# Optimization experiments

Hardware: AMD Instinct MI355X
Metric: run time of the kernel (lower is better)

Reference implementation:

```python
import jax, jax.numpy as jnp
import numpy as np

B = 131072
LATENT, COND = 32, 96
HIDDEN, OUT = 128, 64
E = 8            # num experts
NUM_LAYER = 3    # hidden layer count -> NUM_LAYER+1 expert layers
GH = 128         # gate hidden size
INPUT = LATENT + COND      # 128
INTER = LATENT + HIDDEN    # 160
EPS = 1e-5


def _u(key, shape, stdv):
    return jax.random.uniform(key, shape, jnp.float32, -stdv, stdv)


def setup_inputs() -> dict:
    key = jax.random.key(0)
    ks = jax.random.split(key, 20)
    inp = {
        'z': jax.random.normal(ks[0], (B, LATENT), jnp.float32),
        'c': jax.random.normal(ks[1], (B, COND), jnp.float32),
    }
    # expert layers: (in_dim, out_dim) per layer
    dims = [(INPUT, HIDDEN), (INTER, HIDDEN), (INTER, HIDDEN), (INTER, OUT)]
    for i, (j, k) in enumerate(dims):
        stdv = 1.0 / np.sqrt(j)
        inp[f'w{i}'] = _u(ks[2 + 2 * i], (E, j, k), stdv)
        inp[f'b{i}'] = _u(ks[3 + 2 * i], (E, k), stdv)
    # gate MLP: Linear(INPUT,GH) -> ELU -> Linear(GH,GH) -> ELU -> Linear(GH,E)
    gd = [(INPUT, GH), (GH, GH), (GH, E)]
    for i, (j, k) in enumerate(gd):
        stdv = 1.0 / np.sqrt(j)
        inp[f'gw{i}'] = _u(ks[10 + 2 * i], (j, k), stdv)
        inp[f'gb{i}'] = _u(ks[11 + 2 * i], (k,), stdv)
    return inp


def _layernorm(x):
    # F.layer_norm(x, x.shape[1:]) with no affine params
    mu = jnp.mean(x, axis=-1, keepdims=True)
    var = jnp.mean(jnp.square(x - mu), axis=-1, keepdims=True)
    return (x - mu) * jax.lax.rsqrt(var + EPS)


def reference(z, c, w0, b0, w1, b1, w2, b2, w3, b3,
              gw0, gb0, gw1, gb1, gw2, gb2):
    x = jnp.concatenate([z, c], axis=-1)                      # [B, INPUT]
    h = jax.nn.elu(x @ gw0 + gb0)
    h = jax.nn.elu(h @ gw1 + gb1)
    coeff = jax.nn.softmax(h @ gw2 + gb2, axis=-1)            # [B, E]

    layer_out = c
    layers = [(w0, b0, True), (w1, b1, True), (w2, b2, True), (w3, b3, False)]
    for w, b, act in layers:
        inp = jnp.concatenate([z, layer_out], axis=-1)        # [B, J]
        inp = _layernorm(inp)
        mixed_bias = coeff @ b                                # be,ek->bk
        mixed = jnp.einsum('be,bj,ejk->bk', coeff, inp, w)    # soft-MoE mix
        out = mixed + mixed_bias
        layer_out = jax.nn.elu(out) if act else out
    return layer_out
```

## Files before the change

### kernel.cpp

```cpp
#include <hip/hip_runtime.h>

typedef _Float16 f16;
typedef _Float16 f16x2 __attribute__((ext_vector_type(2)));
typedef _Float16 f16x4 __attribute__((ext_vector_type(4)));
typedef _Float16 f16x8 __attribute__((ext_vector_type(8)));
typedef float f32x16 __attribute__((ext_vector_type(16)));

#define DEV __device__ __forceinline__
#define MFMA16(a, b, cc) __builtin_amdgcn_mfma_f32_32x32x16_f16(a, b, cc, 0, 0, 0)


constexpr int OFF_W0 = 0;
constexpr int OFF_W1 = 131072;
constexpr int OFF_W2 = 294912;
constexpr int OFF_W3 = 458752;
constexpr int OFF_G0 = 540672;
constexpr int OFF_G1 = 557056;
constexpr int OFF_B0 = 573440;
constexpr int OFF_B1 = 575488;
constexpr int OFF_B2 = 577536;
constexpr int OFF_B3 = 579584;

__global__ __launch_bounds__(256) void repack_kernel(
    const float* __restrict__ w0, const float* __restrict__ w1,
    const float* __restrict__ w2, const float* __restrict__ w3,
    const float* __restrict__ gw0, const float* __restrict__ gw1,
    const float* __restrict__ b0, const float* __restrict__ b1,
    const float* __restrict__ b2, const float* __restrict__ b3,
    f16* __restrict__ ws)
{
  int g = blockIdx.x * 256 + threadIdx.x;
  if (g < 71680) {
    const float* src; int S, CT, K, dstoff, lg;
    if (g < 16384)      { src = w0;  S = 8;  CT = 4; K = 128; dstoff = OFF_W0; lg = g; }
    else if (g < 36864) { src = w1;  S = 10; CT = 4; K = 128; dstoff = OFF_W1; lg = g - 16384; }
    else if (g < 57344) { src = w2;  S = 10; CT = 4; K = 128; dstoff = OFF_W2; lg = g - 36864; }
    else if (g < 67584) { src = w3;  S = 10; CT = 2; K = 64;  dstoff = OFF_W3; lg = g - 57344; }
    else if (g < 69632) { src = gw0; S = 8;  CT = 4; K = 128; dstoff = OFF_G0; lg = g - 67584; }
    else                { src = gw1; S = 8;  CT = 4; K = 128; dstoff = OFF_G1; lg = g - 69632; }
    int l = lg & 63;
    int t = lg >> 6;
    int ct = t % CT; t /= CT;
    int s = t % S;
    int e = t / S;
    int J = S * 16;
    int n  = ct * 32 + (l & 31);
    int jb = s * 16 + (l >> 5) * 8;
    f16* dst = ws + dstoff + (size_t)lg * 8;
#pragma unroll
    for (int i = 0; i < 8; ++i)
      dst[i] = (f16)src[((size_t)(e * J + jb + i)) * K + n];
  } else if (g < 72576) {
    int bg = g - 71680;
    const float* src; int K, dstoff, lb;
    if (bg < 256)      { src = b0; K = 128; dstoff = OFF_B0; lb = bg; }
    else if (bg < 512) { src = b1; K = 128; dstoff = OFF_B1; lb = bg - 256; }
    else if (bg < 768) { src = b2; K = 128; dstoff = OFF_B2; lb = bg - 512; }
    else               { src = b3; K = 64;  dstoff = OFF_B3; lb = bg - 768; }
    int l = lb & 63, ct = lb >> 6;
    int n = ct * 32 + (l & 31);
    f16* dst = ws + dstoff + (size_t)lb * 8;
#pragma unroll
    for (int i = 0; i < 8; ++i)
      dst[i] = (l < 32) ? (f16)src[i * K + n] : (f16)0.0f;
  }
}

DEV unsigned char* actsp(unsigned char* acts, int row, int colb) {
  return acts + (((row << 8) + colb) ^ ((row & 15) << 4));
}

DEV f16x8 cvt8(float4 a, float4 b) {
  f16x8 r;
  r[0] = (f16)a.x; r[1] = (f16)a.y; r[2] = (f16)a.z; r[3] = (f16)a.w;
  r[4] = (f16)b.x; r[5] = (f16)b.y; r[6] = (f16)b.z; r[7] = (f16)b.w;
  return r;
}

template <int NF>
DEV void rowstats(const f16x8 (&F)[NF], float invJ, float& mu, float& rs) {
  float s1 = 0.f, s2 = 0.f;
#pragma unroll
  for (int i = 0; i < NF; ++i)
#pragma unroll
    for (int q = 0; q < 8; ++q) {
      float v = (float)F[i][q];
      s1 += v;
      s2 += v * v;
    }
  s1 += __shfl_xor(s1, 32, 64);
  s2 += __shfl_xor(s2, 32, 64);
  mu = s1 * invJ;
  float var = s2 * invJ - mu * mu;
  rs = rsqrtf(var + 1e-5f);
}

template <int NS, int NCTW, int CTTOT, int N16>
DEV void expert_loop(const f16x8 (&F)[NS], float mu, float rs,
                     unsigned char* wb0, unsigned char* wb1,
                     const f16x8 cf,
                     const f16* wsrc, const f16* nextsrc, int next_n16,
                     int ct0, int lane, int tid,
                     f32x16 (&acc)[NCTW]) {
#pragma unroll
  for (int e = 0; e < 8; ++e) {
    unsigned char* rb  = (e & 1) ? wb1 : wb0;
    unsigned char* wbn = (e & 1) ? wb0 : wb1;
    const float4* src = (const float4*)((e < 7) ? (wsrc + (size_t)(e + 1) * N16 * 8) : nextsrc);
    int n16 = (e < 7) ? N16 : next_n16;
    float4 stg[5];
#pragma unroll
    for (int k = 0; k < 5; ++k) {
      int idx = tid + k * 512;
      if (idx < n16) stg[k] = src[idx];
    }
    float pf = rs * (float)cf[e];
    f16 p = (f16)pf, q = (f16)(-mu * pf);
#pragma unroll
    for (int s = 0; s < NS; ++s) {
      f16x8 a = F[s] * p + q;
#pragma unroll
      for (int t = 0; t < NCTW; ++t) {
        f16x8 b = *(const f16x8*)(rb + (size_t)(((s * CTTOT) + (ct0 + t)) * 64 + lane) * 16);
        acc[t] = MFMA16(a, b, acc[t]);
      }
    }
#pragma unroll
    for (int k = 0; k < 5; ++k) {
      int idx = tid + k * 512;
      if (idx < n16) *(float4*)(wbn + (size_t)idx * 16) = stg[k];
    }
    __syncthreads();
  }
}

template <int NCTW>
DEV void bias_mfma(f32x16 (&acc)[NCTW], const f16x8 cf, const f16* pb,
                   int ct0, int lane) {
#pragma unroll
  for (int t = 0; t < NCTW; ++t) {
    f16x8 bb = *(const f16x8*)(pb + (size_t)((ct0 + t) * 64 + lane) * 8);
    acc[t] = MFMA16(cf, bb, acc[t]);
  }
}

template <int NCTW>
DEV void store_acts(const f32x16 (&acc)[NCTW], unsigned char* acts,
                    int wrow, int ct0, int lr, int h) {
#pragma unroll
  for (int t = 0; t < NCTW; ++t) {
    int col = (ct0 + t) * 32 + lr;
#pragma unroll
    for (int r = 0; r < 16; ++r) {
      float v = acc[t][r];
      v = v > 0.f ? v : __expf(v) - 1.f;
      int rowl = (r & 3) + 8 * (r >> 2) + 4 * h;
      *(f16*)actsp(acts, wrow * 32 + rowl, col * 2) = (f16)v;
    }
  }
}

__global__ __launch_bounds__(512, 2) void moe_fused(
    const float* __restrict__ z, const float* __restrict__ c,
    const float* __restrict__ gb0, const float* __restrict__ gb1,
    const float* __restrict__ gw2, const float* __restrict__ gb2,
    const f16* __restrict__ ws, float* __restrict__ out)
{
  __shared__ __align__(16) unsigned char smem[116736];
  unsigned char* wb0  = smem;
  unsigned char* wb1  = smem + 40960;
  unsigned char* acts = smem + 81920;
  f16* coeffH = (f16*)(smem + 114688);

  const int tid  = threadIdx.x;
  const int lane = tid & 63;
  const int wave = tid >> 6;
  const int wrow = wave >> 1, wc = wave & 1;
  const int h = lane >> 5, lr = lane & 31;
  const int brow = blockIdx.x << 7;
  const int lrow = wrow * 32 + lr;
  const int ct0 = wc * 2;

  {
    int row = tid >> 2, q4 = tid & 3;
    const float* zr = z + (size_t)(brow + row) * 32;
    const float* cr = c + (size_t)(brow + row) * 96;
#pragma unroll
    for (int jj = 0; jj < 8; ++jj) {
      int j0 = q4 * 32 + jj * 4;
      float4 v = (j0 < 32) ? *(const float4*)(zr + j0)
                           : *(const float4*)(cr + (j0 - 32));
      f16x4 hv = {(f16)v.x, (f16)v.y, (f16)v.z, (f16)v.w};
      *(f16x4*)actsp(acts, row, j0 * 2) = hv;
    }
  }
  float4 stgA[4];
  {
    const float4* g4 = (const float4*)(ws + OFF_G0);
#pragma unroll
    for (int k = 0; k < 4; ++k) stgA[k] = g4[tid + k * 512];
  }
  __syncthreads();

#pragma unroll
  for (int k = 0; k < 4; ++k) *(float4*)(wb0 + (size_t)(tid + k * 512) * 16) = stgA[k];
  f16x8 FX[8];
#pragma unroll
  for (int s = 0; s < 8; ++s)
    FX[s] = *(const f16x8*)actsp(acts, lrow, s * 32 + h * 16);
  float muX, rsX;
  rowstats<8>(FX, 1.f / 128.f, muX, rsX);
  {
    const float4* g4 = (const float4*)(ws + OFF_G1);
#pragma unroll
    for (int k = 0; k < 4; ++k) stgA[k] = g4[tid + k * 512];
  }
  __syncthreads();

  f32x16 acc[2];
#pragma unroll
  for (int t = 0; t < 2; ++t)
#pragma unroll
    for (int i = 0; i < 16; ++i) acc[t][i] = 0.f;
#pragma unroll
  for (int s = 0; s < 8; ++s) {
    f16x8 b0 = *(const f16x8*)(wb0 + (size_t)((s * 4 + ct0) * 64 + lane) * 16);
    f16x8 b1 = *(const f16x8*)(wb0 + (size_t)((s * 4 + ct0 + 1) * 64 + lane) * 16);
    acc[0] = MFMA16(FX[s], b0, acc[0]);
    acc[1] = MFMA16(FX[s], b1, acc[1]);
  }
#pragma unroll
  for (int t = 0; t < 2; ++t) {
    int col = (ct0 + t) * 32 + lr;
    float bias = gb0[col];
#pragma unroll
    for (int r = 0; r < 16; ++r) {
      float v = acc[t][r] + bias;
      v = v > 0.f ? v : __expf(v) - 1.f;
      int rowl = (r & 3) + 8 * (r >> 2) + 4 * h;
      *(f16*)actsp(acts, wrow * 32 + rowl, col * 2) = (f16)v;
    }
  }
#pragma unroll
  for (int k = 0; k < 4; ++k) *(float4*)(wb1 + (size_t)(tid + k * 512) * 16) = stgA[k];
  __syncthreads();

#pragma unroll
  for (int t = 0; t < 2; ++t)
#pragma unroll
    for (int i = 0; i < 16; ++i) acc[t][i] = 0.f;
#pragma unroll
  for (int s = 0; s < 8; ++s) {
    f16x8 a = *(const f16x8*)actsp(acts, lrow, s * 32 + h * 16);
    f16x8 b0 = *(const f16x8*)(wb1 + (size_t)((s * 4 + ct0) * 64 + lane) * 16);
    f16x8 b1 = *(const f16x8*)(wb1 + (size_t)((s * 4 + ct0 + 1) * 64 + lane) * 16);
    acc[0] = MFMA16(a, b0, acc[0]);
    acc[1] = MFMA16(a, b1, acc[1]);
  }
  {
    const float4* g4 = (const float4*)(ws + OFF_W0);
#pragma unroll
    for (int k = 0; k < 4; ++k) stgA[k] = g4[tid + k * 512];
  }
  __syncthreads();
#pragma unroll
  for (int t = 0; t < 2; ++t) {
    int col = (ct0 + t) * 32 + lr;
    float bias = gb1[col];
#pragma unroll
    for (int r = 0; r < 16; ++r) {
      float v = acc[t][r] + bias;
      v = v > 0.f ? v : __expf(v) - 1.f;
      int rowl = (r & 3) + 8 * (r >> 2) + 4 * h;
      *(f16*)actsp(acts, wrow * 32 + rowl, col * 2) = (f16)v;
    }
  }
#pragma unroll
  for (int k = 0; k < 4; ++k) *(float4*)(wb0 + (size_t)(tid + k * 512) * 16) = stgA[k];
  __syncthreads();

  {
    int row = tid >> 2, part = tid & 3;
    float lgt[8];
#pragma unroll
    for (int e = 0; e < 8; ++e) lgt[e] = 0.f;
#pragma unroll
    for (int qq = 0; qq < 4; ++qq) {
      f16x8 hv = *(const f16x8*)actsp(acts, row, part * 64 + qq * 16);
#pragma unroll
      for (int i = 0; i < 8; ++i) {
        float hf = (float)hv[i];
        int j = part * 32 + qq * 8 + i;
        const float4* gp = (const float4*)(gw2 + j * 8);
        float4 ga = gp[0], gb = gp[1];
        lgt[0] += hf * ga.x; lgt[1] += hf * ga.y; lgt[2] += hf * ga.z; lgt[3] += hf * ga.w;
        lgt[4] += hf * gb.x; lgt[5] += hf * gb.y; lgt[6] += hf * gb.z; lgt[7] += hf * gb.w;
      }
    }
#pragma unroll
    for (int e = 0; e < 8; ++e) {
      lgt[e] += __shfl_xor(lgt[e], 1, 64);
      lgt[e] += __shfl_xor(lgt[e], 2, 64);
      lgt[e] += gb2[e];
    }
    float m = lgt[0];
#pragma unroll
    for (int e = 1; e < 8; ++e) m = fmaxf(m, lgt[e]);
    float ssum = 0.f, pe[8];
#pragma unroll
    for (int e = 0; e < 8; ++e) { pe[e] = __expf(lgt[e] - m); ssum += pe[e]; }
    float inv = 1.f / ssum;
    if (part == 0) {
      f16x8 ch;
#pragma unroll
      for (int e = 0; e < 8; ++e) ch[e] = (f16)(pe[e] * inv);
      *(f16x8*)(coeffH + row * 8) = ch;
    }
  }
  __syncthreads();

  const f16x8 cf = *(const f16x8*)(coeffH + lrow * 8);

#pragma unroll
  for (int t = 0; t < 2; ++t)
#pragma unroll
    for (int i = 0; i < 16; ++i) acc[t][i] = 0.f;
  expert_loop<8, 2, 4, 2048>(FX, muX, rsX, wb0, wb1, cf,
                             ws + OFF_W0, ws + OFF_W1, 2560,
                             ct0, lane, tid, acc);
  bias_mfma<2>(acc, cf, ws + OFF_B0, ct0, lane);
  store_acts<2>(acc, acts, wrow, ct0, lr, h);
  __syncthreads();

  f16x8 F[10];
  float mu, rs;
  auto load_layer_frags = [&]() {
#pragma unroll
    for (int s = 0; s < 2; ++s) {
      const float* zp = z + (size_t)(brow + lrow) * 32 + s * 16 + h * 8;
      float4 a0 = *(const float4*)zp, a1 = *(const float4*)(zp + 4);
      F[s] = cvt8(a0, a1);
    }
#pragma unroll
    for (int s = 0; s < 8; ++s)
      F[2 + s] = *(const f16x8*)actsp(acts, lrow, s * 32 + h * 16);
    rowstats<10>(F, 1.f / 160.f, mu, rs);
  };

  load_layer_frags();
#pragma unroll
  for (int t = 0; t < 2; ++t)
#pragma unroll
    for (int i = 0; i < 16; ++i) acc[t][i] = 0.f;
  expert_loop<10, 2, 4, 2560>(F, mu, rs, wb0, wb1, cf,
                              ws + OFF_W1, ws + OFF_W2, 2560,
                              ct0, lane, tid, acc);
  bias_mfma<2>(acc, cf, ws + OFF_B1, ct0, lane);
  store_acts<2>(acc, acts, wrow, ct0, lr, h);
  __syncthreads();

  load_layer_frags();
#pragma unroll
  for (int t = 0; t < 2; ++t)
#pragma unroll
    for (int i = 0; i < 16; ++i) acc[t][i] = 0.f;
  expert_loop<10, 2, 4, 2560>(F, mu, rs, wb0, wb1, cf,
                              ws + OFF_W2, ws + OFF_W3, 1280,
                              ct0, lane, tid, acc);
  bias_mfma<2>(acc, cf, ws + OFF_B2, ct0, lane);
  store_acts<2>(acc, acts, wrow, ct0, lr, h);
  __syncthreads();

  load_layer_frags();
  f32x16 acc3[1];
#pragma unroll
  for (int i = 0; i < 16; ++i) acc3[0][i] = 0.f;
  expert_loop<10, 1, 2, 1280>(F, mu, rs, wb0, wb1, cf,
                              ws + OFF_W3, ws , 0,
                              wc, lane, tid, acc3);
  bias_mfma<1>(acc3, cf, ws + OFF_B3, wc, lane);
  {
    int col = wc * 32 + lr;
#pragma unroll
    for (int r = 0; r < 16; ++r) {
      int rowl = (r & 3) + 8 * (r >> 2) + 4 * h;
      int grow = brow + wrow * 32 + rowl;
      out[(size_t)grow * 64 + col] = acc3[0][r];
    }
  }
}

extern "C" void kernel_launch(void* const* d_in, const int* in_sizes, int n_in,
                              void* d_out, int out_size, void* d_ws, size_t ws_size,
                              hipStream_t stream) {
  (void)in_sizes; (void)n_in; (void)out_size; (void)ws_size;
  const float* z   = (const float*)d_in[0];
  const float* c   = (const float*)d_in[1];
  const float* w0  = (const float*)d_in[2];
  const float* b0  = (const float*)d_in[3];
  const float* w1  = (const float*)d_in[4];
  const float* b1  = (const float*)d_in[5];
  const float* w2  = (const float*)d_in[6];
  const float* b2  = (const float*)d_in[7];
  const float* w3  = (const float*)d_in[8];
  const float* b3  = (const float*)d_in[9];
  const float* gw0 = (const float*)d_in[10];
  const float* gb0 = (const float*)d_in[11];
  const float* gw1 = (const float*)d_in[12];
  const float* gb1 = (const float*)d_in[13];
  const float* gw2 = (const float*)d_in[14];
  const float* gb2 = (const float*)d_in[15];
  f16* ws = (f16*)d_ws;
  float* out = (float*)d_out;

  repack_kernel<<<dim3(284), dim3(256), 0, stream>>>(
      w0, w1, w2, w3, gw0, gw1, b0, b1, b2, b3, ws);
  moe_fused<<<dim3(1024), dim3(512), 0, stream>>>(
      z, c, gb0, gb1, gw2, gb2, ws, out);
}
```

Before: 501.0 us.

## Use 4 waves per block with each wave computing all output columns

Changes the block from 8 waves (4 row groups × 2 column halves) to 4 waves. Each wave now covers a 32-row slab across all output column tiles, so every A fragment is reused over 4 MFMAs instead of 2 and the redundant per-wave normalization and fragment loads disappear. Weight staging per thread doubles, raising register pressure, and launch bounds change to (256,1), which allows fewer concurrent waves per CU to hide latency. LDS usage per block is unchanged, so occupancy is likely limited to about 1 block of 4 waves per SIMD group.

```diff
diff --git a/kernel.cpp b/kernel.cpp
--- a/kernel.cpp
+++ b/kernel.cpp
@@ -100,7 +100,7 @@
                      unsigned char* wb0, unsigned char* wb1,
                      const f16x8 cf,
                      const f16* wsrc, const f16* nextsrc, int next_n16,
-                     int ct0, int lane, int tid,
+                     int lane, int tid,
                      f32x16 (&acc)[NCTW]) {
 #pragma unroll
   for (int e = 0; e < 8; ++e) {
@@ -108,10 +108,10 @@
     unsigned char* wbn = (e & 1) ? wb0 : wb1;
     const float4* src = (const float4*)((e < 7) ? (wsrc + (size_t)(e + 1) * N16 * 8) : nextsrc);
     int n16 = (e < 7) ? N16 : next_n16;
-    float4 stg[5];
-#pragma unroll
-    for (int k = 0; k < 5; ++k) {
-      int idx = tid + k * 512;
+    float4 stg[10];
+#pragma unroll
+    for (int k = 0; k < 10; ++k) {
+      int idx = tid + k * 256;
       if (idx < n16) stg[k] = src[idx];
     }
     float pf = rs * (float)cf[e];
@@ -121,13 +121,13 @@
       f16x8 a = F[s] * p + q;
 #pragma unroll
       for (int t = 0; t < NCTW; ++t) {
-        f16x8 b = *(const f16x8*)(rb + (size_t)(((s * CTTOT) + (ct0 + t)) * 64 + lane) * 16);
+        f16x8 b = *(const f16x8*)(rb + (size_t)(((s * CTTOT) + t) * 64 + lane) * 16);
         acc[t] = MFMA16(a, b, acc[t]);
       }
     }
 #pragma unroll
-    for (int k = 0; k < 5; ++k) {
-      int idx = tid + k * 512;
+    for (int k = 0; k < 10; ++k) {
+      int idx = tid + k * 256;
       if (idx < n16) *(float4*)(wbn + (size_t)idx * 16) = stg[k];
     }
     __syncthreads();
@@ -135,32 +135,31 @@
 }
 
 template <int NCTW>
-DEV void bias_mfma(f32x16 (&acc)[NCTW], const f16x8 cf, const f16* pb,
-                   int ct0, int lane) {
+DEV void bias_mfma(f32x16 (&acc)[NCTW], const f16x8 cf, const f16* pb, int lane) {
 #pragma unroll
   for (int t = 0; t < NCTW; ++t) {
-    f16x8 bb = *(const f16x8*)(pb + (size_t)((ct0 + t) * 64 + lane) * 8);
+    f16x8 bb = *(const f16x8*)(pb + (size_t)(t * 64 + lane) * 8);
     acc[t] = MFMA16(cf, bb, acc[t]);
   }
 }
 
 template <int NCTW>
 DEV void store_acts(const f32x16 (&acc)[NCTW], unsigned char* acts,
-                    int wrow, int ct0, int lr, int h) {
+                    int wave, int lr, int h) {
 #pragma unroll
   for (int t = 0; t < NCTW; ++t) {
-    int col = (ct0 + t) * 32 + lr;
+    int col = t * 32 + lr;
 #pragma unroll
     for (int r = 0; r < 16; ++r) {
       float v = acc[t][r];
       v = v > 0.f ? v : __expf(v) - 1.f;
       int rowl = (r & 3) + 8 * (r >> 2) + 4 * h;
-      *(f16*)actsp(acts, wrow * 32 + rowl, col * 2) = (f16)v;
-    }
-  }
-}
-
-__global__ __launch_bounds__(512, 2) void moe_fused(
+      *(f16*)actsp(acts, wave * 32 + rowl, col * 2) = (f16)v;
+    }
+  }
+}
+
+__global__ __launch_bounds__(256, 1) void moe_fused(
     const float* __restrict__ z, const float* __restrict__ c,
     const float* __restrict__ gb0, const float* __restrict__ gb1,
     const float* __restrict__ gw2, const float* __restrict__ gb2,
@@ -175,35 +174,33 @@
   const int tid  = threadIdx.x;
   const int lane = tid & 63;
   const int wave = tid >> 6;
-  const int wrow = wave >> 1, wc = wave & 1;
   const int h = lane >> 5, lr = lane & 31;
   const int brow = blockIdx.x << 7;
-  const int lrow = wrow * 32 + lr;
-  const int ct0 = wc * 2;
+  const int lrow = wave * 32 + lr;
 
   {
-    int row = tid >> 2, q4 = tid & 3;
+    int row = tid >> 1, half = tid & 1;
     const float* zr = z + (size_t)(brow + row) * 32;
     const float* cr = c + (size_t)(brow + row) * 96;
 #pragma unroll
-    for (int jj = 0; jj < 8; ++jj) {
-      int j0 = q4 * 32 + jj * 4;
+    for (int jj = 0; jj < 16; ++jj) {
+      int j0 = half * 64 + jj * 4;
       float4 v = (j0 < 32) ? *(const float4*)(zr + j0)
                            : *(const float4*)(cr + (j0 - 32));
       f16x4 hv = {(f16)v.x, (f16)v.y, (f16)v.z, (f16)v.w};
       *(f16x4*)actsp(acts, row, j0 * 2) = hv;
     }
   }
-  float4 stgA[4];
+  float4 stgA[8];
   {
     const float4* g4 = (const float4*)(ws + OFF_G0);
 #pragma unroll
-    for (int k = 0; k < 4; ++k) stgA[k] = g4[tid + k * 512];
-  }
-  __syncthreads();
-
-#pragma unroll
-  for (int k = 0; k < 4; ++k) *(float4*)(wb0 + (size_t)(tid + k * 512) * 16) = stgA[k];
+    for (int k = 0; k < 8; ++k) stgA[k] = g4[tid + k * 256];
+  }
+  __syncthreads();
+
+#pragma unroll
+  for (int k = 0; k < 8; ++k) *(float4*)(wb0 + (size_t)(tid + k * 256) * 16) = stgA[k];
   f16x8 FX[8];
 #pragma unroll
   for (int s = 0; s < 8; ++s)
@@ -213,84 +210,93 @@
   {
     const float4* g4 = (const float4*)(ws + OFF_G1);
 #pragma unroll
-    for (int k = 0; k < 4; ++k) stgA[k] = g4[tid + k * 512];
-  }
-  __syncthreads();
-
-  f32x16 acc[2];
-#pragma unroll
-  for (int t = 0; t < 2; ++t)
+    for (int k = 0; k < 8; ++k) stgA[k] = g4[tid + k * 256];
+  }
+  __syncthreads();
+
+  f32x16 acc[4];
+#pragma unroll
+  for (int t = 0; t < 4; ++t)
 #pragma unroll
     for (int i = 0; i < 16; ++i) acc[t][i] = 0.f;
 #pragma unroll
   for (int s = 0; s < 8; ++s) {
-    f16x8 b0 = *(const f16x8*)(wb0 + (size_t)((s * 4 + ct0) * 64 + lane) * 16);
-    f16x8 b1 = *(const f16x8*)(wb0 + (size_t)((s * 4 + ct0 + 1) * 64 + lane) * 16);
-    acc[0] = MFMA16(FX[s], b0, acc[0]);
-    acc[1] = MFMA16(FX[s], b1, acc[1]);
-  }
-#pragma unroll
-  for (int t = 0; t < 2; ++t) {
-    int col = (ct0 + t) * 32 + lr;
+#pragma unroll
+    for (int t = 0; t < 4; ++t) {
+      f16x8 b = *(const f16x8*)(wb0 + (size_t)((s * 4 + t) * 64 + lane) * 16);
+      acc[t] = MFMA16(FX[s], b, acc[t]);
+    }
+  }
+#pragma unroll
+  for (int t = 0; t < 4; ++t) {
+    int col = t * 32 + lr;
     float bias = gb0[col];
 #pragma unroll
     for (int r = 0; r < 16; ++r) {
       float v = acc[t][r] + bias;
       v = v > 0.f ? v : __expf(v) - 1.f;
       int rowl = (r & 3) + 8 * (r >> 2) + 4 * h;
-      *(f16*)actsp(acts, wrow * 32 + rowl, col * 2) = (f16)v;
-    }
-  }
-#pragma unroll
-  for (int k = 0; k < 4; ++k) *(float4*)(wb1 + (size_t)(tid + k * 512) * 16) = stgA[k];
-  __syncthreads();
-
-#pragma unroll
-  for (int t = 0; t < 2; ++t)
+      *(f16*)actsp(acts, wave * 32 + rowl, col * 2) = (f16)v;
+    }
+  }
+#pragma unroll
+  for (int k = 0; k < 8; ++k) *(float4*)(wb1 + (size_t)(tid + k * 256) * 16) = stgA[k];
+  __syncthreads();
+
+#pragma unroll
+  for (int t = 0; t < 4; ++t)
 #pragma unroll
     for (int i = 0; i < 16; ++i) acc[t][i] = 0.f;
 #pragma unroll
   for (int s = 0; s < 8; ++s) {
     f16x8 a = *(const f16x8*)actsp(acts, lrow, s * 32 + h * 16);
-    f16x8 b0 = *(const f16x8*)(wb1 + (size_t)((s * 4 + ct0) * 64 + lane) * 16);
-    f16x8 b1 = *(const f16x8*)(wb1 + (size_t)((s * 4 + ct0 + 1) * 64 + lane) * 16);
-    acc[0] = MFMA16(a, b0, acc[0]);
-    acc[1] = MFMA16(a, b1, acc[1]);
-  }
+#pragma unroll
+    for (int t = 0; t < 4; ++t) {
+      f16x8 b = *(const f16x8*)(wb1 + (size_t)((s * 4 + t) * 64 + lane) * 16);
+      acc[t] = MFMA16(a, b, acc[t]);
+    }
+  }
+  float4 stgW[10];
   {
     const float4* g4 = (const float4*)(ws + OFF_W0);
 #pragma unroll
-    for (int k = 0; k < 4; ++k) stgA[k] = g4[tid + k * 512];
-  }
-  __syncthreads();
-#pragma unroll
-  for (int t = 0; t < 2; ++t) {
-    int col = (ct0 + t) * 32 + lr;
+    for (int k = 0; k < 10; ++k) {
+      int idx = tid + k * 256;
+      if (idx < 2048) stgW[k] = g4[idx];
+    }
+  }
+  __syncthreads();
+#pragma unroll
+  for (int t = 0; t < 4; ++t) {
+    int col = t * 32 + lr;
     float bias = gb1[col];
 #pragma unroll
     for (int r = 0; r < 16; ++r) {
       float v = acc[t][r] + bias;
       v = v > 0.f ? v : __expf(v) - 1.f;
       int rowl = (r & 3) + 8 * (r >> 2) + 4 * h;
-      *(f16*)actsp(acts, wrow * 32 + rowl, col * 2) = (f16)v;
-    }
-  }
-#pragma unroll
-  for (int k = 0; k < 4; ++k) *(float4*)(wb0 + (size_t)(tid + k * 512) * 16) = stgA[k];
+      *(f16*)actsp(acts, wave * 32 + rowl, col * 2) = (f16)v;
+    }
+  }
+#pragma unroll
+  for (int k = 0; k < 10; ++k) {
+    int idx = tid + k * 256;
+    if (idx < 2048) *(float4*)(wb0 + (size_t)idx * 16) = stgW[k];
+  }
   __syncthreads();
 
   {
-    int row = tid >> 2, part = tid & 3;
+    int row = tid >> 1, part = tid & 1;
     float lgt[8];
 #pragma unroll
     for (int e = 0; e < 8; ++e) lgt[e] = 0.f;
 #pragma unroll
-    for (int qq = 0; qq < 4; ++qq) {
-      f16x8 hv = *(const f16x8*)actsp(acts, row, part * 64 + qq * 16);
+    for (int qq = 0; qq < 8; ++qq) {
+      f16x8 hv = *(const f16x8*)actsp(acts, row, part * 128 + qq * 16);
 #pragma unroll
       for (int i = 0; i < 8; ++i) {
         float hf = (float)hv[i];
-        int j = part * 32 + qq * 8 + i;
+        int j = part * 64 + qq * 8 + i;
         const float4* gp = (const float4*)(gw2 + j * 8);
         float4 ga = gp[0], gb = gp[1];
         lgt[0] += hf * ga.x; lgt[1] += hf * ga.y; lgt[2] += hf * ga.z; lgt[3] += hf * ga.w;
@@ -300,7 +306,6 @@
 #pragma unroll
     for (int e = 0; e < 8; ++e) {
       lgt[e] += __shfl_xor(lgt[e], 1, 64);
-      lgt[e] += __shfl_xor(lgt[e], 2, 64);
       lgt[e] += gb2[e];
     }
     float m = lgt[0];
@@ -322,14 +327,14 @@
   const f16x8 cf = *(const f16x8*)(coeffH + lrow * 8);
 
 #pragma unroll
-  for (int t = 0; t < 2; ++t)
+  for (int t = 0; t < 4; ++t)
 #pragma unroll
     for (int i = 0; i < 16; ++i) acc[t][i] = 0.f;
-  expert_loop<8, 2, 4, 2048>(FX, muX, rsX, wb0, wb1, cf,
+  expert_loop<8, 4, 4, 2048>(FX, muX, rsX, wb0, wb1, cf,
                              ws + OFF_W0, ws + OFF_W1, 2560,
-                             ct0, lane, tid, acc);
-  bias_mfma<2>(acc, cf, ws + OFF_B0, ct0, lane);
-  store_acts<2>(acc, acts, wrow, ct0, lr, h);
+                             lane, tid, acc);
+  bias_mfma<4>(acc, cf, ws + OFF_B0, lane);
+  store_acts<4>(acc, acts, wave, lr, h);
   __syncthreads();
 
   f16x8 F[10];
@@ -349,43 +354,46 @@
 
   load_layer_frags();
 #pragma unroll
+  for (int t = 0; t < 4; ++t)
+#pragma unroll
+    for (int i = 0; i < 16; ++i) acc[t][i] = 0.f;
+  expert_loop<10, 4, 4, 2560>(F, mu, rs, wb0, wb1, cf,
+                              ws + OFF_W1, ws + OFF_W2, 2560,
+                              lane, tid, acc);
+  bias_mfma<4>(acc, cf, ws + OFF_B1, lane);
+  store_acts<4>(acc, acts, wave, lr, h);
+  __syncthreads();
+
+  load_layer_frags();
+#pragma unroll
+  for (int t = 0; t < 4; ++t)
+#pragma unroll
+    for (int i = 0; i < 16; ++i) acc[t][i] = 0.f;
+  expert_loop<10, 4, 4, 2560>(F, mu, rs, wb0, wb1, cf,
+                              ws + OFF_W2, ws + OFF_W3, 1280,
+                              lane, tid, acc);
+  bias_mfma<4>(acc, cf, ws + OFF_B2, lane);
+  store_acts<4>(acc, acts, wave, lr, h);
+  __syncthreads();
+
+  load_layer_frags();
+  f32x16 acc3[2];
+#pragma unroll
   for (int t = 0; t < 2; ++t)
 #pragma unroll
-    for (int i = 0; i < 16; ++i) acc[t][i] = 0.f;
-  expert_loop<10, 2, 4, 2560>(F, mu, rs, wb0, wb1, cf,
-                              ws + OFF_W1, ws + OFF_W2, 2560,
-                              ct0, lane, tid, acc);
-  bias_mfma<2>(acc, cf, ws + OFF_B1, ct0, lane);
-  store_acts<2>(acc, acts, wrow, ct0, lr, h);
-  __syncthreads();
-
-  load_layer_frags();
-#pragma unroll
-  for (int t = 0; t < 2; ++t)
-#pragma unroll
-    for (int i = 0; i < 16; ++i) acc[t][i] = 0.f;
-  expert_loop<10, 2, 4, 2560>(F, mu, rs, wb0, wb1, cf,
-                              ws + OFF_W2, ws + OFF_W3, 1280,
-                              ct0, lane, tid, acc);
-  bias_mfma<2>(acc, cf, ws + OFF_B2, ct0, lane);
-  store_acts<2>(acc, acts, wrow, ct0, lr, h);
-  __syncthreads();
-
-  load_layer_frags();
-  f32x16 acc3[1];
-#pragma unroll
-  for (int i = 0; i < 16; ++i) acc3[0][i] = 0.f;
-  expert_loop<10, 1, 2, 1280>(F, mu, rs, wb0, wb1, cf,
+    for (int i = 0; i < 16; ++i) acc3[t][i] = 0.f;
+  expert_loop<10, 2, 2, 1280>(F, mu, rs, wb0, wb1, cf,
                               ws + OFF_W3, ws , 0,
-                              wc, lane, tid, acc3);
-  bias_mfma<1>(acc3, cf, ws + OFF_B3, wc, lane);
-  {
-    int col = wc * 32 + lr;
+                              lane, tid, acc3);
+  bias_mfma<2>(acc3, cf, ws + OFF_B3, lane);
+#pragma unroll
+  for (int t = 0; t < 2; ++t) {
+    int col = t * 32 + lr;
 #pragma unroll
     for (int r = 0; r < 16; ++r) {
       int rowl = (r & 3) + 8 * (r >> 2) + 4 * h;
-      int grow = brow + wrow * 32 + rowl;
-      out[(size_t)grow * 64 + col] = acc3[0][r];
+      int grow = brow + wave * 32 + rowl;
+      out[(size_t)grow * 64 + col] = acc3[t][r];
     }
   }
 }
@@ -415,6 +423,6 @@
 
   repack_kernel<<<dim3(284), dim3(256), 0, stream>>>(
       w0, w1, w2, w3, gw0, gw1, b0, b1, b2, b3, ws);
-  moe_fused<<<dim3(1024), dim3(512), 0, stream>>>(
+  moe_fused<<<dim3(1024), dim3(256), 0, stream>>>(
       z, c, gb0, gb1, gw2, gb2, ws, out);
 }
```

Measured after the change: 618.0 us. +23.4%, slower.
